# Optimization experiments

Measured on AMD Instinct MI355X. Metric: run time of the kernel, lower is better.

The kernel has to match this reference:

```python
import jax, jax.numpy as jnp
import numpy as np

N_NODES, N_FEATS, HIDDEN, N_CLASS = 100000, 256, 128, 64
B, K0, K1, N_HIST = 1024, 25, 10, 5


def setup_inputs() -> dict:
    key = jax.random.key(0)
    ks = jax.random.split(key, 11)
    return {
        "feats": jax.random.normal(ks[0], (N_NODES, N_FEATS), dtype=jnp.float32),
        "history": jax.random.normal(ks[1], (N_NODES, HIDDEN), dtype=jnp.float32),
        "W0": jax.random.normal(ks[2], (2 * N_FEATS, HIDDEN), dtype=jnp.float32) * 0.05,
        "b0": jax.random.normal(ks[3], (HIDDEN,), dtype=jnp.float32) * 0.05,
        "W1": jax.random.normal(ks[4], (2 * HIDDEN, N_CLASS), dtype=jnp.float32) * 0.05,
        "b1": jax.random.normal(ks[5], (N_CLASS,), dtype=jnp.float32) * 0.05,
        "nodes": jax.random.randint(ks[6], (B,), 0, N_NODES, dtype=jnp.int64 if jax.config.jax_enable_x64 else jnp.int32),
        "neighs0": jax.random.randint(ks[7], (B, K0), 0, N_NODES),
        "neighs1": jax.random.randint(ks[8], (B, K1), 0, N_NODES),
        "neighs0_nb": jax.random.randint(ks[9], (B * K1, K0), 0, N_NODES),
        "h_nodes": jax.random.randint(ks[10], (B, N_HIST), 0, N_NODES),
    }


def _layer0(feats, W0, b0, h_prev, neighs):
    # h_prev: [M, 1, F]; neighs: [M, K0]
    neigh_feats = feats[neighs]                       # [M, K0, F] gather
    h = jnp.mean(neigh_feats, axis=1, keepdims=True)  # MeanAggregator -> [M, 1, F]
    h = jnp.concatenate([h_prev, h], axis=-1)         # [M, 1, 2F]
    return jax.nn.relu(h @ W0 + b0)                   # [M, 1, H]


def reference(feats, history, W0, b0, W1, b1, nodes, neighs0, neighs1, neighs0_nb, h_nodes):
    # ---- layer 0 for the seed nodes (x = feats[nodes], detached per source) ----
    x = jax.lax.stop_gradient(feats[nodes])           # torch: x.detach().clone()
    h_prev = x[:, None, :]                            # [B, 1, F]
    h1 = _layer0(feats, W0, b0, h_prev, neighs0)      # [B, 1, H]

    # ---- layer 1: recursive layer-0 embeddings of sampled neighbors ----
    nx = jax.lax.stop_gradient(feats[neighs1.reshape(-1)])[:, None, :]  # [B*K1, 1, F]
    neigh_original = _layer0(feats, W0, b0, nx, neighs0_nb)             # [B*K1, 1, H]
    neigh_original = neigh_original.reshape(B, K1, HIDDEN)

    # historical-activation trick (history lookups are detached in source)
    neigh_historical = jax.lax.stop_gradient(history[h_nodes])          # [B, 5, H]
    neigh_delta = neigh_original - jax.lax.stop_gradient(history[neighs1])
    neigh_delta = neigh_delta * (N_HIST / K1)
    neigh_feats = jnp.concatenate([neigh_delta, neigh_historical], axis=1)  # [B, K1+5, H]
    # NOTE: source also scatters history[neighs1] = neigh_original (side effect);
    # functional equivalent: history.at[neighs1].set(neigh_original), not returned here.

    h = jnp.mean(neigh_feats, axis=1, keepdims=True)                    # [B, 1, H]
    h = jnp.concatenate([h1, h], axis=-1)                               # [B, 1, 2H]
    h = jax.nn.relu(h @ W1 + b1)                                        # [B, 1, C]
    return h.squeeze(1)                                                 # [B, C]
```

## Files before the change

### kernel.cpp

```cpp
#include <hip/hip_runtime.h>

#define N_FEATS 256
#define HIDDEN  128
#define N_CLASS 64
#define BATCH   1024
#define K0      25
#define K1      10
#define N_HIST  5
#define M_TOTAL (BATCH + BATCH * K1)
#define KDIM    512
#define N_NODES 100000

typedef unsigned short u16;
typedef short bf16x8 __attribute__((ext_vector_type(8)));
typedef _Float16 f16x8 __attribute__((ext_vector_type(8)));
typedef float f32x4 __attribute__((ext_vector_type(4)));

static __device__ __forceinline__ u16 f2bf(float f) {
    union { float f; unsigned int i; } v;
    v.f = f;
    unsigned int x = v.i;
    x += ((x >> 16) & 1u) + 0x7FFFu;
    return (u16)(x >> 16);
}
static __device__ __forceinline__ unsigned int pack2(float lo, float hi) {
    return (unsigned int)f2bf(lo) | ((unsigned int)f2bf(hi) << 16);
}
static __device__ __forceinline__ u16 f2h(float f) {
    union { _Float16 h; u16 u; } v;
    v.h = (_Float16)f;
    return v.u;
}
static __device__ __forceinline__ int loadI(const void* p, long long i, int f64) {
    const char* cp = (const char*)p + (f64 ? (i << 3) : (i << 2));
    return *(const int*)cp;
}

__global__ void k_detect(const void* __restrict__ nodes, int* __restrict__ flag) {
    if (threadIdx.x == 0 && blockIdx.x == 0) {
        const int* p = (const int*)nodes;
        int f = 1;
        for (int i = 0; i < 8; ++i)
            if (p[2 * i + 1] != 0) f = 0;
        *flag = f;
    }
}


__global__ void k_transpose_w0h(const float* __restrict__ W0, u16* __restrict__ W0T2,
                                const void* __restrict__ nodes, int* __restrict__ flag) {
    if (threadIdx.x == 0 && threadIdx.y == 0 && blockIdx.x == 0 && blockIdx.y == 0) {
        const int* p = (const int*)nodes;
        int f = 1;
        for (int i = 0; i < 8; ++i)
            if (p[2 * i + 1] != 0) f = 0;
        *flag = f;
    }
    __shared__ u16 tile[32][33];
    int tx = threadIdx.x;
    int ty = threadIdx.y;
    int k0 = blockIdx.x * 32;
    int n0 = blockIdx.y * 32;
#pragma unroll
    for (int i = 0; i < 32; i += 8)
        tile[ty + i][tx] = f2h(W0[(size_t)(k0 + ty + i) * HIDDEN + n0 + tx]);
    __syncthreads();
    int roff = (k0 >= 256) ? 128 : 0;
    int kk = k0 & 255;
#pragma unroll
    for (int i = 0; i < 32; i += 8)
        W0T2[(size_t)(n0 + ty + i + roff) * 256 + kk + tx] = tile[tx][ty + i];
}

#define TROWS      32
#define NTILES     3125
#define BOT_NBLK   768
__global__ __launch_bounds__(512, 6) void k_projbot(
        const float* __restrict__ feats,
        const u16* __restrict__ W0T2,
        u16* __restrict__ Pb) {
    __shared__ u16 Xs[2][TROWS][256 + 8];
    const int tid = threadIdx.x;
    const int wv = tid >> 6;
    const int lane = tid & 63;
    const int m = lane & 15;
    const int q = lane >> 4;
    const int base = NTILES / BOT_NBLK;
    const int rem = NTILES - base * BOT_NBLK;
    const int bi = blockIdx.x;
    const int s0 = bi * base + (bi < rem ? bi : rem);
    const int cnt = base + (bi < rem ? 1 : 0);

    f16x8 B0[8];
    {
        const u16* bb = W0T2 + (size_t)(128 + wv * 16 + m) * 256 + q * 8;
#pragma unroll
        for (int kk = 0; kk < 8; ++kk)
            B0[kk] = *(const f16x8*)(bb + kk * 32);
    }

    float4 st[4];
    const float* fbase = feats + (size_t)(wv * 4) * N_FEATS + lane * 4;

#define PROJ_ISSUE(t)                                                         \
    {                                                                         \
        const float* fp_ = fbase + (size_t)(t) * (TROWS * N_FEATS);           \
        _Pragma("unroll")                                                     \
        for (int i = 0; i < 4; ++i)                                           \
            st[i] = *(const float4*)(fp_ + (size_t)i * N_FEATS);              \
    }
#define PROJ_WRITE(b)                                                         \
    {                                                                         \
        _Pragma("unroll")                                                     \
        for (int i = 0; i < 4; ++i) {                                         \
            ushort4 pk;                                                       \
            pk.x = f2h(st[i].x); pk.y = f2h(st[i].y);                         \
            pk.z = f2h(st[i].z); pk.w = f2h(st[i].w);                         \
            *(ushort4*)&Xs[b][wv * 4 + i][lane * 4] = pk;                     \
        }                                                                     \
    }

    PROJ_ISSUE(s0);
    PROJ_WRITE(0);
    PROJ_ISSUE(s0 + 1);
    __syncthreads();

    int cur = 0;
    for (int tt = 0; tt < cnt; ++tt) {
        const int t = s0 + tt;
        f32x4 a0 = (f32x4){0.f,0.f,0.f,0.f};
        f32x4 a1 = (f32x4){0.f,0.f,0.f,0.f};
#pragma unroll
        for (int kk = 0; kk < 8; ++kk) {
            f16x8 f0 = *(const f16x8*)&Xs[cur][m][kk * 32 + q * 8];
            f16x8 f1 = *(const f16x8*)&Xs[cur][m + 16][kk * 32 + q * 8];
            a0 = __builtin_amdgcn_mfma_f32_16x16x32_f16(f0, B0[kk], a0, 0, 0, 0);
            a1 = __builtin_amdgcn_mfma_f32_16x16x32_f16(f1, B0[kk], a1, 0, 0, 0);
        }
        __syncthreads();
#pragma unroll
        for (int r = 0; r < 4; ++r) {
            Xs[cur][q * 4 + r][wv * 16 + m]      = f2h(a0[r]);
            Xs[cur][16 + q * 4 + r][wv * 16 + m] = f2h(a1[r]);
        }
        if (tt + 1 < cnt) {
            PROJ_WRITE(cur ^ 1);
            if (tt + 2 < cnt) PROJ_ISSUE(t + 2);
        }
        __syncthreads();
        {
            const int row0 = tid >> 4;
            const int c8 = (tid & 15) * 8;
            uint4 w = *(const uint4*)&Xs[cur][row0][c8];
            *(uint4*)(Pb + (size_t)(t * TROWS + row0) * 128 + c8) = w;
        }
        cur ^= 1;
    }
#undef PROJ_ISSUE
#undef PROJ_WRITE
}

__global__ __launch_bounds__(512) void k_top(
        const float* __restrict__ feats,
        const void* __restrict__ nodes,
        const void* __restrict__ neighs1,
        const u16* __restrict__ W0T2,
        u16* __restrict__ Htop,
        const int* __restrict__ flag) {
    __shared__ u16 Xs[16][256 + 8];
    const int f64 = *flag;
    int wv = threadIdx.x >> 6;
    int lane = threadIdx.x & 63;
    int row0 = blockIdx.x * 16;
    int d = lane * 4;

#pragma unroll
    for (int i = 0; i < 2; ++i) {
        int lr = wv * 2 + i;
        int g = row0 + lr;
        int selfIdx = (g < BATCH) ? loadI(nodes, g, f64)
                                  : loadI(neighs1, g - BATCH, f64);
        float4 sv = *(const float4*)(feats + (size_t)selfIdx * N_FEATS + d);
        ushort4 pk;
        pk.x = f2h(sv.x); pk.y = f2h(sv.y); pk.z = f2h(sv.z); pk.w = f2h(sv.w);
        *(ushort4*)&Xs[lr][d] = pk;
    }
    __syncthreads();

    int m = lane & 15;
    int q = lane >> 4;
    f32x4 acc = (f32x4){0.f, 0.f, 0.f, 0.f};
    const u16* bbase = W0T2 + (size_t)(wv * 16 + m) * 256 + q * 8;
#pragma unroll
    for (int kk = 0; kk < 8; ++kk) {
        f16x8 af = *(const f16x8*)&Xs[m][kk * 32 + q * 8];
        f16x8 bf = *(const f16x8*)(bbase + kk * 32);
        acc = __builtin_amdgcn_mfma_f32_16x16x32_f16(af, bf, acc, 0, 0, 0);
    }
    int col = wv * 16 + m;
#pragma unroll
    for (int r = 0; r < 4; ++r)
        Htop[(size_t)(row0 + q * 4 + r) * 128 + col] = f2h(acc[r]);
}

__global__ __launch_bounds__(256) void k_gf(
        const u16* __restrict__ Pb,
        const u16* __restrict__ Htop,
        const float* __restrict__ history,
        const void* __restrict__ neighs0,
        const void* __restrict__ neighs1,
        const void* __restrict__ neighs0_nb,
        const void* __restrict__ h_nodes,
        const float* __restrict__ b0,
        const float* __restrict__ W1,
        const float* __restrict__ b1,
        float* __restrict__ out,
        const int* __restrict__ flag) {
    __shared__ float Hs[11][128];
    __shared__ float hcat[2 * HIDDEN];
    __shared__ float red[256];
    const int f64 = *flag;
    const int tid = threadIdx.x;
    const int b = blockIdx.x;
    const int wv = tid >> 6;
    const int lane = tid & 63;
    const int m = lane & 15;
    const int grp = lane >> 4;

    for (int r = wv; r < 11; r += 4) {
        const void* nbp;
        long long nbo;
        int g;
        if (r == 0) {
            nbp = neighs0; nbo = (long long)b * K0; g = b;
        } else {
            int rr = b * K1 + (r - 1);
            nbp = neighs0_nb; nbo = (long long)rr * K0; g = BATCH + rr;
        }
        int idx[K0];
#pragma unroll
        for (int k = 0; k < K0; ++k) idx[k] = loadI(nbp, nbo + k, f64);

        float a[8];
#pragma unroll
        for (int i = 0; i < 8; ++i) a[i] = 0.f;
#pragma unroll
        for (int k = 0; k < 7; ++k) {
            int k1 = 4 * k + grp;
            if (k1 < K0) {
                f16x8 v = *(const f16x8*)(Pb + (size_t)idx[k1] * 128 + m * 8);
#pragma unroll
                for (int i = 0; i < 8; ++i) a[i] += (float)v[i];
            }
        }
#pragma unroll
        for (int i = 0; i < 8; ++i) {
            a[i] += __shfl_xor(a[i], 16);
            a[i] += __shfl_xor(a[i], 32);
        }
        if (grp == 0) {
            f16x8 sv = *(const f16x8*)(Htop + (size_t)g * 128 + m * 8);
            const float inv = 1.0f / (float)K0;
#pragma unroll
            for (int i = 0; i < 8; ++i) {
                float y = a[i] * inv + (float)sv[i] + b0[m * 8 + i];
                Hs[r][m * 8 + i] = y > 0.f ? y : 0.f;
            }
        }
    }
    __syncthreads();

    const int j = tid & 127;
    const int half = tid >> 7;
    float S = 0.f;
    if (half == 0) hcat[j] = Hs[0][j];
#pragma unroll
    for (int t = half * 5; t < half * 5 + 5; ++t) {
        int n1 = loadI(neighs1, b * K1 + t, f64);
        S += 0.5f * (Hs[1 + t][j] - history[(size_t)n1 * HIDDEN + j]);
    }
    if (half == 1) {
#pragma unroll
        for (int u = 0; u < N_HIST; ++u) {
            int hn = loadI(h_nodes, b * N_HIST + u, f64);
            S += history[(size_t)hn * HIDDEN + j];
        }
    }
    red[tid] = S;
    __syncthreads();
    if (half == 0)
        hcat[HIDDEN + j] = (red[j] + red[HIDDEN + j]) * (1.0f / 15.0f);
    __syncthreads();

    const int n = tid & 63;
    const int seg = tid >> 6;
    float p = 0.f;
#pragma unroll 8
    for (int i = seg * 64; i < seg * 64 + 64; ++i)
        p += hcat[i] * W1[(size_t)i * N_CLASS + n];
    red[tid] = p;
    __syncthreads();
    if (tid < 64) {
        float a = red[tid] + red[tid + 64] + red[tid + 128] + red[tid + 192]
                + b1[tid];
        a = a > 0.f ? a : 0.f;
        out[(size_t)b * N_CLASS + tid] = a;
    }
}

__global__ void k_transpose_w0(const float* __restrict__ W0, u16* __restrict__ W0T) {
    __shared__ u16 tile[32][33];
    int tx = threadIdx.x;
    int ty = threadIdx.y;
    int k0 = blockIdx.x * 32;
    int n0 = blockIdx.y * 32;
#pragma unroll
    for (int i = 0; i < 32; i += 8)
        tile[ty + i][tx] = f2bf(W0[(size_t)(k0 + ty + i) * HIDDEN + n0 + tx]);
    __syncthreads();
#pragma unroll
    for (int i = 0; i < 32; i += 8)
        W0T[(size_t)(n0 + ty + i) * KDIM + k0 + tx] = tile[tx][ty + i];
}

__global__ __launch_bounds__(512) void k_layer0(
        const float* __restrict__ feats,
        const void* __restrict__ nodes,
        const void* __restrict__ neighs0,
        const void* __restrict__ neighs1,
        const void* __restrict__ neighs0_nb,
        const u16* __restrict__ W0T,
        const float* __restrict__ b0,
        float* __restrict__ H,
        const int* __restrict__ flag) {
    __shared__ u16 Xs[16][KDIM + 8];
    const int f64 = *flag;
    int wv = threadIdx.x >> 6;
    int lane = threadIdx.x & 63;
    int row0 = blockIdx.x * 16;
    int d = lane * 4;

#pragma unroll
    for (int i = 0; i < 2; ++i) {
        int lr = wv * 2 + i;
        int g = row0 + lr;
        int selfIdx;
        const void* nbp;
        long long nbo;
        if (g < BATCH) {
            selfIdx = loadI(nodes, g, f64);
            nbp = neighs0; nbo = (long long)g * K0;
        } else {
            int rr = g - BATCH;
            selfIdx = loadI(neighs1, rr, f64);
            nbp = neighs0_nb; nbo = (long long)rr * K0;
        }
        int idx[K0];
#pragma unroll
        for (int k = 0; k < K0; ++k) idx[k] = loadI(nbp, nbo + k, f64);

        float4 sv = *(const float4*)(feats + (size_t)selfIdx * N_FEATS + d);
        float a0 = 0.f, a1 = 0.f, a2 = 0.f, a3 = 0.f;
#pragma unroll
        for (int k = 0; k < K0; ++k) {
            float4 v = *(const float4*)(feats + (size_t)idx[k] * N_FEATS + d);
            a0 += v.x; a1 += v.y; a2 += v.z; a3 += v.w;
        }
        const float inv = 1.0f / (float)K0;
        uint2 spk, mpk;
        spk.x = pack2(sv.x, sv.y);
        spk.y = pack2(sv.z, sv.w);
        mpk.x = pack2(a0 * inv, a1 * inv);
        mpk.y = pack2(a2 * inv, a3 * inv);
        *(uint2*)&Xs[lr][d] = spk;
        *(uint2*)&Xs[lr][N_FEATS + d] = mpk;
    }
    __syncthreads();

    int m = lane & 15;
    int q = lane >> 4;
    f32x4 acc = (f32x4){0.f, 0.f, 0.f, 0.f};
    const u16* bbase = W0T + (size_t)(wv * 16 + m) * KDIM + q * 8;
#pragma unroll
    for (int k0 = 0; k0 < KDIM; k0 += 32) {
        bf16x8 af = *(const bf16x8*)&Xs[m][k0 + q * 8];
        bf16x8 bf = *(const bf16x8*)(bbase + k0);
        acc = __builtin_amdgcn_mfma_f32_16x16x32_bf16(af, bf, acc, 0, 0, 0);
    }
    int col = wv * 16 + m;
    float bias = b0[col];
#pragma unroll
    for (int r = 0; r < 4; ++r) {
        float y = acc[r] + bias;
        y = y > 0.f ? y : 0.f;
        H[(size_t)(row0 + q * 4 + r) * HIDDEN + col] = y;
    }
}

__global__ __launch_bounds__(256) void k_final(
        const float* __restrict__ H,
        const float* __restrict__ history,
        const void* __restrict__ neighs1,
        const void* __restrict__ h_nodes,
        const float* __restrict__ W1,
        const float* __restrict__ b1,
        float* __restrict__ out,
        const int* __restrict__ flag) {
    __shared__ float hcat[2 * HIDDEN];
    __shared__ float red[256];
    const int f64 = *flag;
    const int tid = threadIdx.x;
    const int b = blockIdx.x;
    const int j = tid & 127;
    const int half = tid >> 7;

    float S = 0.f;
    if (half == 0) hcat[j] = H[(size_t)b * HIDDEN + j];
#pragma unroll
    for (int t = half * 5; t < half * 5 + 5; ++t) {
        float orig = H[(size_t)(BATCH + b * K1 + t) * HIDDEN + j];
        int n1 = loadI(neighs1, b * K1 + t, f64);
        float hist = history[(size_t)n1 * HIDDEN + j];
        S += 0.5f * (orig - hist);
    }
    if (half == 1) {
#pragma unroll
        for (int u = 0; u < N_HIST; ++u) {
            int hn = loadI(h_nodes, b * N_HIST + u, f64);
            S += history[(size_t)hn * HIDDEN + j];
        }
    }
    red[tid] = S;
    __syncthreads();
    if (half == 0)
        hcat[HIDDEN + j] = (red[j] + red[HIDDEN + j]) * (1.0f / 15.0f);
    __syncthreads();

    const int n = tid & 63;
    const int seg = tid >> 6;
    float p = 0.f;
#pragma unroll 8
    for (int i = seg * 64; i < seg * 64 + 64; ++i)
        p += hcat[i] * W1[(size_t)i * N_CLASS + n];
    red[tid] = p;
    __syncthreads();
    if (tid < 64) {
        float a = red[tid] + red[tid + 64] + red[tid + 128] + red[tid + 192]
                + b1[tid];
        a = a > 0.f ? a : 0.f;
        out[(size_t)b * N_CLASS + tid] = a;
    }
}

static __device__ __forceinline__ float loadF_m(const void* p, long long i, int fbf) {
    const char* cp = (const char*)p + (fbf ? (i << 1) : (i << 2));
    if (fbf) {
        union { unsigned int u; float f; } v;
        v.u = ((unsigned int)(*(const u16*)cp)) << 16;
        return v.f;
    }
    return *(const float*)cp;
}

__global__ __launch_bounds__(256) void k_fused(
        const void* __restrict__ feats,
        const void* __restrict__ history,
        const void* __restrict__ W0,
        const void* __restrict__ b0,
        const void* __restrict__ W1,
        const void* __restrict__ b1,
        const void* __restrict__ nodes,
        const void* __restrict__ neighs0,
        const void* __restrict__ neighs1,
        const void* __restrict__ neighs0_nb,
        const void* __restrict__ h_nodes,
        float* __restrict__ out) {
    __shared__ float W0s[32][128];
    __shared__ float Xs[11][KDIM];
    __shared__ float hcat[2 * HIDDEN];
    __shared__ float red[256];
    __shared__ int ibuf[K0 + 1];
    __shared__ int sflags[2];

    const int tid = threadIdx.x;
    const int b = blockIdx.x;

    if (tid == 0) {
        const int* ip = (const int*)nodes;
        int f = 1;
        for (int i = 0; i < 8; ++i)
            if (ip[2 * i + 1] != 0) f = 0;
        sflags[0] = f;
        const u16* qp = (const u16*)feats;
        int cnt = 0;
        for (int i = 0; i < 64; ++i) {
            int e = (qp[2 * i] >> 7) & 0xFF;
            if (e >= 90 && e <= 134) cnt++;
        }
        sflags[1] = (cnt >= 40) ? 1 : 0;
    }
    __syncthreads();
    const int f64 = sflags[0];
    const int fbf = sflags[1];

    for (int r = 0; r < 11; ++r) {
        __syncthreads();
        if (tid < K0) {
            long long nbo = (r == 0) ? ((long long)b * K0)
                                     : ((long long)(b * K1 + (r - 1)) * K0);
            const void* nbp = (r == 0) ? neighs0 : neighs0_nb;
            ibuf[tid] = loadI(nbp, nbo + tid, f64);
        } else if (tid == K0) {
            ibuf[K0] = (r == 0) ? loadI(nodes, b, f64)
                                : loadI(neighs1, b * K1 + (r - 1), f64);
        }
        __syncthreads();
        int sidx = ibuf[K0];
        Xs[r][tid] = loadF_m(feats, (long long)sidx * N_FEATS + tid, fbf);
        float s = 0.f;
#pragma unroll
        for (int k = 0; k < K0; ++k)
            s += loadF_m(feats, (long long)ibuf[k] * N_FEATS + tid, fbf);
        Xs[r][N_FEATS + tid] = s * (1.0f / (float)K0);
    }
    __syncthreads();

    const int c = tid & 127;
    const int ph = tid >> 7;
    float acc[11];
#pragma unroll
    for (int r = 0; r < 11; ++r) acc[r] = 0.f;

    for (int s = 0; s < 16; ++s) {
        __syncthreads();
#pragma unroll
        for (int i = 0; i < 16; ++i) {
            int idx = tid + 256 * i;
            int k = idx >> 7, cc = idx & 127;
            W0s[k][cc] = loadF_m(W0, (long long)(32 * s + k) * HIDDEN + cc, fbf);
        }
        __syncthreads();
        const int kb = 32 * s + 16 * ph;
#pragma unroll
        for (int r = 0; r < 11; ++r) {
            float a = 0.f;
#pragma unroll
            for (int j = 0; j < 16; ++j)
                a += Xs[r][kb + j] * W0s[16 * ph + j][c];
            acc[r] += a;
        }
    }

    float S = 0.f;
    float b0v = (tid < 128) ? loadF_m(b0, tid, fbf) : 0.f;
    for (int r = 0; r < 11; ++r) {
        __syncthreads();
        red[tid] = acc[r];
        __syncthreads();
        if (tid < 128) {
            float h = red[tid] + red[tid + 128] + b0v;
            h = h > 0.f ? h : 0.f;
            if (r == 0) {
                hcat[tid] = h;
            } else {
                int n1 = loadI(neighs1, b * K1 + (r - 1), f64);
                float hist = loadF_m(history, (long long)n1 * HIDDEN + tid, fbf);
                S += 0.5f * (h - hist);
            }
        }
    }
    if (tid < 128) {
#pragma unroll
        for (int u = 0; u < N_HIST; ++u) {
            int hn = loadI(h_nodes, b * N_HIST + u, f64);
            S += loadF_m(history, (long long)hn * HIDDEN + tid, fbf);
        }
        hcat[HIDDEN + tid] = S * (1.0f / 15.0f);
    }
    __syncthreads();

    const int n = tid & 63;
    const int seg = tid >> 6;
    float p = 0.f;
#pragma unroll 8
    for (int i = seg * 64; i < seg * 64 + 64; ++i)
        p += hcat[i] * loadF_m(W1, (long long)i * N_CLASS + n, fbf);
    red[tid] = p;
    __syncthreads();
    if (tid < 64) {
        float a = red[tid] + red[tid + 64] + red[tid + 128] + red[tid + 192]
                + loadF_m(b1, tid, fbf);
        a = a > 0.f ? a : 0.f;
        out[(long long)b * N_CLASS + tid] = a;
    }
}

extern "C" void kernel_launch(void* const* d_in, const int* in_sizes, int n_in,
                              void* d_out, int out_size, void* d_ws, size_t ws_size,
                              hipStream_t stream) {
    (void)out_size;
    const long long want[11] = {25600000, 12800000, 65536, 128, 16384, 64,
                                1024, 25600, 10240, 256000, 5120};
    const void* bp[11];
    for (int j = 0; j < 11; ++j) bp[j] = d_in[j < n_in ? j : 0];
    for (int j = 0; j < 11; ++j) {
        if (j < n_in && (long long)in_sizes[j] == want[j]) continue;
        for (int i = 0; i < n_in; ++i)
            if ((long long)in_sizes[i] == want[j]) { bp[j] = d_in[i]; break; }
    }

    const size_t PB_BYTES = (size_t)N_NODES * 128 * 2;
    const size_t HT_BYTES = (size_t)M_TOTAL * 128 * 2;
    const size_t OFF_PB   = 131072;
    const size_t OFF_HT   = OFF_PB + PB_BYTES;
    const size_t OFF_FLAG = OFF_HT + HT_BYTES;
    const size_t WS_NEW   = OFF_FLAG + 16;
    const size_t WS_OLD  = 131072 + 5767168 + 16;

    if (ws_size >= WS_NEW) {
        char* ws = (char*)d_ws;
        u16* W0T2 = (u16*)ws;
        u16* Pb   = (u16*)(ws + OFF_PB);
        u16* Htop = (u16*)(ws + OFF_HT);
        int* flag = (int*)(ws + OFF_FLAG);

        k_transpose_w0h<<<dim3(16, 4), dim3(32, 8), 0, stream>>>(
            (const float*)bp[2], W0T2, bp[6], flag);
        k_projbot<<<BOT_NBLK, 512, 0, stream>>>((const float*)bp[0], W0T2, Pb);
        k_top<<<M_TOTAL / 16, 512, 0, stream>>>(
            (const float*)bp[0], bp[6], bp[8], W0T2, Htop, flag);
        k_gf<<<BATCH, 256, 0, stream>>>(
            Pb, Htop, (const float*)bp[1], bp[7], bp[8], bp[9], bp[10],
            (const float*)bp[3], (const float*)bp[4], (const float*)bp[5],
            (float*)d_out, flag);
        return;
    }

    if (ws_size >= WS_OLD) {
        char* ws = (char*)d_ws;
        u16* W0T  = (u16*)ws;
        float* H  = (float*)(ws + 131072);
        int* flag = (int*)(ws + 131072 + 5767168);

        k_detect<<<1, 1, 0, stream>>>(bp[6], flag);
        k_transpose_w0<<<dim3(16, 4), dim3(32, 8), 0, stream>>>((const float*)bp[2], W0T);
        k_layer0<<<M_TOTAL / 16, 512, 0, stream>>>(
            (const float*)bp[0], bp[6], bp[7], bp[8], bp[9], W0T,
            (const float*)bp[3], H, flag);
        k_final<<<BATCH, 256, 0, stream>>>(
            H, (const float*)bp[1], bp[8], bp[10],
            (const float*)bp[4], (const float*)bp[5], (float*)d_out, flag);
        return;
    }

    k_fused<<<BATCH, 256, 0, stream>>>(
        bp[0], bp[1], bp[2], bp[3], bp[4], bp[5],
        bp[6], bp[7], bp[8], bp[9], bp[10], (float*)d_out);
}
```

Measured before the change: 58.51 us.

## Restructure bottom projection to per-wave 16-row tiles with shared W0 in LDS

```diff
diff --git a/kernel.cpp b/kernel.cpp
--- a/kernel.cpp
+++ b/kernel.cpp
@@ -72,92 +72,86 @@
         W0T2[(size_t)(n0 + ty + i + roff) * 256 + kk + tx] = tile[tx][ty + i];
 }
 
-#define TROWS      32
-#define NTILES     3125
-#define BOT_NBLK   768
-__global__ __launch_bounds__(512, 6) void k_projbot(
+#define BOT2_NBLK  256
+#define BOT2_WAVES (BOT2_NBLK * 8)
+#define NT16       (N_NODES / 16)
+__global__ __launch_bounds__(512) void k_projbot2(
         const float* __restrict__ feats,
         const u16* __restrict__ W0T2,
         u16* __restrict__ Pb) {
-    __shared__ u16 Xs[2][TROWS][256 + 8];
+    __shared__ u16 Bs[128][264];
+    __shared__ u16 Xs[8][16][264];
     const int tid = threadIdx.x;
     const int wv = tid >> 6;
     const int lane = tid & 63;
     const int m = lane & 15;
     const int q = lane >> 4;
-    const int base = NTILES / BOT_NBLK;
-    const int rem = NTILES - base * BOT_NBLK;
-    const int bi = blockIdx.x;
-    const int s0 = bi * base + (bi < rem ? bi : rem);
-    const int cnt = base + (bi < rem ? 1 : 0);
-
-    f16x8 B0[8];
-    {
-        const u16* bb = W0T2 + (size_t)(128 + wv * 16 + m) * 256 + q * 8;
-#pragma unroll
-        for (int kk = 0; kk < 8; ++kk)
-            B0[kk] = *(const f16x8*)(bb + kk * 32);
-    }
-
-    float4 st[4];
-    const float* fbase = feats + (size_t)(wv * 4) * N_FEATS + lane * 4;
-
-#define PROJ_ISSUE(t)                                                         \
+
+#pragma unroll
+    for (int i = 0; i < 8; ++i) {
+        int idx = tid + i * 512;
+        int r = idx >> 5;
+        int c = (idx & 31) * 8;
+        *(uint4*)&Bs[r][c] = *(const uint4*)(W0T2 + (size_t)(128 + r) * 256 + c);
+    }
+
+    const int w0 = blockIdx.x * 8 + wv;
+    float4 sA[16], sB[16];
+
+#define B2_ISSUE(S, t)                                                        \
     {                                                                         \
-        const float* fp_ = fbase + (size_t)(t) * (TROWS * N_FEATS);           \
+        const float* fp_ = feats + (size_t)(t) * (16 * N_FEATS) + lane * 4;   \
         _Pragma("unroll")                                                     \
-        for (int i = 0; i < 4; ++i)                                           \
-            st[i] = *(const float4*)(fp_ + (size_t)i * N_FEATS);              \
-    }
-#define PROJ_WRITE(b)                                                         \
+        for (int i = 0; i < 16; ++i)                                          \
+            S[i] = *(const float4*)(fp_ + (size_t)i * N_FEATS);               \
+    }
+#define B2_WRITE(S)                                                           \
     {                                                                         \
         _Pragma("unroll")                                                     \
-        for (int i = 0; i < 4; ++i) {                                         \
+        for (int i = 0; i < 16; ++i) {                                        \
             ushort4 pk;                                                       \
-            pk.x = f2h(st[i].x); pk.y = f2h(st[i].y);                         \
-            pk.z = f2h(st[i].z); pk.w = f2h(st[i].w);                         \
-            *(ushort4*)&Xs[b][wv * 4 + i][lane * 4] = pk;                     \
+            pk.x = f2h(S[i].x); pk.y = f2h(S[i].y);                           \
+            pk.z = f2h(S[i].z); pk.w = f2h(S[i].w);                           \
+            *(ushort4*)&Xs[wv][i][lane * 4] = pk;                             \
         }                                                                     \
     }
 
-    PROJ_ISSUE(s0);
-    PROJ_WRITE(0);
-    PROJ_ISSUE(s0 + 1);
-    __syncthreads();
-
-    int cur = 0;
-    for (int tt = 0; tt < cnt; ++tt) {
-        const int t = s0 + tt;
-        f32x4 a0 = (f32x4){0.f,0.f,0.f,0.f};
-        f32x4 a1 = (f32x4){0.f,0.f,0.f,0.f};
+    if (w0 < NT16) B2_ISSUE(sA, w0);
+    __syncthreads();
+
+    int useA = 1;
+    for (int t = w0; t < NT16; t += BOT2_WAVES) {
+        const int nxt = t + BOT2_WAVES;
+        if (useA) {
+            B2_WRITE(sA);
+            if (nxt < NT16) B2_ISSUE(sB, nxt);
+        } else {
+            B2_WRITE(sB);
+            if (nxt < NT16) B2_ISSUE(sA, nxt);
+        }
+        useA ^= 1;
+
+        f32x4 acc[8];
+#pragma unroll
+        for (int nt = 0; nt < 8; ++nt) acc[nt] = (f32x4){0.f, 0.f, 0.f, 0.f};
 #pragma unroll
         for (int kk = 0; kk < 8; ++kk) {
-            f16x8 f0 = *(const f16x8*)&Xs[cur][m][kk * 32 + q * 8];
-            f16x8 f1 = *(const f16x8*)&Xs[cur][m + 16][kk * 32 + q * 8];
-            a0 = __builtin_amdgcn_mfma_f32_16x16x32_f16(f0, B0[kk], a0, 0, 0, 0);
-            a1 = __builtin_amdgcn_mfma_f32_16x16x32_f16(f1, B0[kk], a1, 0, 0, 0);
-        }
-        __syncthreads();
-#pragma unroll
-        for (int r = 0; r < 4; ++r) {
-            Xs[cur][q * 4 + r][wv * 16 + m]      = f2h(a0[r]);
-            Xs[cur][16 + q * 4 + r][wv * 16 + m] = f2h(a1[r]);
-        }
-        if (tt + 1 < cnt) {
-            PROJ_WRITE(cur ^ 1);
-            if (tt + 2 < cnt) PROJ_ISSUE(t + 2);
-        }
-        __syncthreads();
-        {
-            const int row0 = tid >> 4;
-            const int c8 = (tid & 15) * 8;
-            uint4 w = *(const uint4*)&Xs[cur][row0][c8];
-            *(uint4*)(Pb + (size_t)(t * TROWS + row0) * 128 + c8) = w;
-        }
-        cur ^= 1;
-    }
-#undef PROJ_ISSUE
-#undef PROJ_WRITE
+            f16x8 af = *(const f16x8*)&Xs[wv][m][kk * 32 + q * 8];
+#pragma unroll
+            for (int nt = 0; nt < 8; ++nt) {
+                f16x8 bf = *(const f16x8*)&Bs[nt * 16 + m][kk * 32 + q * 8];
+                acc[nt] = __builtin_amdgcn_mfma_f32_16x16x32_f16(af, bf, acc[nt], 0, 0, 0);
+            }
+        }
+        u16* prow = Pb + (size_t)(t * 16 + q * 4) * 128 + m;
+#pragma unroll
+        for (int nt = 0; nt < 8; ++nt)
+#pragma unroll
+            for (int r = 0; r < 4; ++r)
+                prow[(size_t)r * 128 + nt * 16] = f2h(acc[nt][r]);
+    }
+#undef B2_ISSUE
+#undef B2_WRITE
 }
 
 __global__ __launch_bounds__(512) void k_top(
@@ -626,7 +620,7 @@
 
         k_transpose_w0h<<<dim3(16, 4), dim3(32, 8), 0, stream>>>(
             (const float*)bp[2], W0T2, bp[6], flag);
-        k_projbot<<<BOT_NBLK, 512, 0, stream>>>((const float*)bp[0], W0T2, Pb);
+        k_projbot2<<<BOT2_NBLK, 512, 0, stream>>>((const float*)bp[0], W0T2, Pb);
         k_top<<<M_TOTAL / 16, 512, 0, stream>>>(
             (const float*)bp[0], bp[6], bp[8], W0T2, Htop, flag);
         k_gf<<<BATCH, 256, 0, stream>>>(
```

Result: slower. 64.02 us (+9.4%).
